# Kernel tuning notes

Measured on AMD Instinct MI355X. Metric: run time of the kernel, lower is better.

## Reference

```python
import jax, jax.numpy as jnp
import numpy as np

N, K, D, VOCAB = 20000, 32, 128, 100000
NEG = -1e30  # finite large-negative so all-masked rows don't produce NaN softmax


def setup_inputs() -> dict:
    key = jax.random.key(0)
    ks = jax.random.split(key, 10)
    return {
        "nodes": jax.random.randint(ks[0], (N,), 0, VOCAB),
        "neigh_idx": jax.random.randint(ks[1], (N, K), 0, VOCAB),
        "neigh_len": jax.random.randint(ks[2], (N,), 0, K + 1),
        "u2e": jax.random.normal(ks[3], (VOCAB, D), dtype=jnp.float32),
        "W1": jax.random.normal(ks[4], (D, 2 * D), dtype=jnp.float32) * 0.05,
        "b1": jax.random.normal(ks[5], (D,), dtype=jnp.float32) * 0.05,
        "W2": jax.random.normal(ks[6], (D, D), dtype=jnp.float32) * 0.05,
        "b2": jax.random.normal(ks[7], (D,), dtype=jnp.float32) * 0.05,
        "W3": jax.random.normal(ks[8], (1, D), dtype=jnp.float32) * 0.05,
        "b3": jax.random.normal(ks[9], (1,), dtype=jnp.float32) * 0.05,
    }


def reference(nodes, neigh_idx, neigh_len, u2e, W1, b1, W2, b2, W3, b3):
    # self features: [N, D]
    self_feats = u2e[nodes]
    # neighbor features gather: [N, K, D]
    e_u = u2e[neigh_idx]
    # GraphRec Attention: cat(neighbor, self-broadcast) -> MLP -> softmax over K
    x = jnp.concatenate(
        [e_u, jnp.broadcast_to(self_feats[:, None, :], e_u.shape)], axis=-1
    )  # [N, K, 2D]
    h = jax.nn.relu(jnp.einsum("nkf,df->nkd", x, W1) + b1)
    h = jax.nn.relu(jnp.einsum("nkd,ed->nke", h, W2) + b2)
    logits = jnp.einsum("nkd,od->nko", h, W3)[..., 0] + b3[0]  # [N, K]
    mask = jnp.arange(K)[None, :] < neigh_len[:, None]  # [N, K]
    att = jax.nn.softmax(jnp.where(mask, logits, NEG), axis=1)
    att = jnp.where(mask, att, 0.0)  # zero out padded slots (and all-empty rows)
    # attention-weighted neighbor aggregation: [N, D]
    agg = jnp.einsum("nk,nkd->nd", att, e_u)
    has_neigh = (neigh_len > 0)[:, None]
    return jnp.where(has_neigh, (agg + self_feats) * 0.5, self_feats)
```

## Files before the change

kernel.cpp:

```cpp
#include <hip/hip_runtime.h>
#include <hip/hip_bf16.h>
#include <stdint.h>

#define KN 32
#define D  128
#define NNODES 20000
#define GRID 2500
#define ITERS 4
#define VOCAB 100000
#define SV1_BLOCKS ((NNODES + 127) / 128)

typedef __bf16 bf16;
typedef __bf16 bf16x8 __attribute__((ext_vector_type(8)));
typedef float  f32x4  __attribute__((ext_vector_type(4)));

#define CHUNK_E 520
#define EU_NODE_E (8 * CHUNK_E)
#define H_STRIDE 136

#define GL2LDS(src, dst) __builtin_amdgcn_global_load_lds(                 \
    (const __attribute__((address_space(1))) void*)(src),                  \
    (__attribute__((address_space(3))) void*)(dst), 16, 0, 0)

#define MFMA(a, b, c) __builtin_amdgcn_mfma_f32_16x16x32_bf16((a), (b), (c), 0, 0, 0)

__global__ __launch_bounds__(256) void pack_weights_kernel(
    const float* __restrict__ W1, const float* __restrict__ W2,
    bf16* __restrict__ w1p, bf16* __restrict__ w2p)
{
    int t = blockIdx.x * 256 + threadIdx.x;
    if (t < 32768) {
        int j = t & 7, lane = (t >> 3) & 63, kt = (t >> 9) & 7, nt = t >> 12;
        int d = nt * 16 + (lane & 15);
        int f = kt * 32 + ((lane >> 4) << 3) + j;
        w1p[t] = (bf16)W1[d * 256 + f];
    } else if (t < 49152) {
        int u = t - 32768;
        int j = u & 7, lane = (u >> 3) & 63, kt = (u >> 9) & 3, nt = u >> 11;
        int e  = nt * 16 + (lane & 15);
        int dd = kt * 32 + ((lane >> 4) << 3) + j;
        w2p[u] = (bf16)W2[e * 128 + dd];
    }
}

__global__ __launch_bounds__(256) void convert_table_kernel(
    const float* __restrict__ u2e, bf16* __restrict__ tbl)
{
    size_t i = ((size_t)blockIdx.x * 256 + threadIdx.x) * 8;
    float4 a = *(const float4*)(u2e + i);
    float4 b = *(const float4*)(u2e + i + 4);
    bf16x8 v;
    v[0]=(bf16)a.x; v[1]=(bf16)a.y; v[2]=(bf16)a.z; v[3]=(bf16)a.w;
    v[4]=(bf16)b.x; v[5]=(bf16)b.y; v[6]=(bf16)b.z; v[7]=(bf16)b.w;
    *(bf16x8*)(tbl + i) = v;
}

__global__ __launch_bounds__(256) void sv1_kernel(
    const int*  __restrict__ nodes,
    const bf16* __restrict__ u2e_bf,
    const bf16* __restrict__ w1p,
    float*      __restrict__ sv1t)
{
    __shared__ alignas(16) bf16 sr[4 * EU_NODE_E];

    const int t    = threadIdx.x;
    const int lane = t & 63;
    const int wave = t >> 6;
    const int ln15 = lane & 15;
    const int quad = lane >> 4;
    const int r0   = blockIdx.x * 128;

    #pragma unroll
    for (int c = 0; c < 8; ++c) {
        int grow = r0 + wave * 32 + c + ((lane >> 4) << 3);
        int node = nodes[grow < NNODES ? grow : NNODES - 1];
        GL2LDS(u2e_bf + (size_t)node * D + ((lane & 15) << 3),
               sr + wave * EU_NODE_E + c * CHUNK_E);
    }
    __syncthreads();

    const bf16* g  = sr + wave * EU_NODE_E;
    const int   rb = (ln15 & 7) * CHUNK_E + (ln15 >> 3) * 128;

    #pragma unroll 1
    for (int np = 0; np < 4; ++np) {
        int nt0 = np * 2;
        bf16x8 b0[4], b1[4];
        #pragma unroll
        for (int kt = 0; kt < 4; ++kt) {
            b0[kt] = *(const bf16x8*)(w1p + (nt0 * 8 + 4 + kt) * 512 + lane * 8);
            b1[kt] = *(const bf16x8*)(w1p + ((nt0 + 1) * 8 + 4 + kt) * 512 + lane * 8);
        }
        f32x4 c00 = {0.f,0.f,0.f,0.f}, c01 = c00, c10 = c00, c11 = c00;
        #pragma unroll
        for (int kt = 0; kt < 4; ++kt) {
            bf16x8 a0 = *(const bf16x8*)(g + rb + kt * 32 + quad * 8);
            bf16x8 a1 = *(const bf16x8*)(g + rb + 256 + kt * 32 + quad * 8);
            c00 = MFMA(a0, b0[kt], c00);
            c01 = MFMA(a0, b1[kt], c01);
            c10 = MFMA(a1, b0[kt], c10);
            c11 = MFMA(a1, b1[kt], c11);
        }
        #pragma unroll
        for (int r = 0; r < 4; ++r) {
            int row = quad * 4 + r;
            int gr0 = r0 + wave * 32 + row;
            int gr1 = gr0 + 16;
            if (gr0 < NNODES) {
                sv1t[(size_t)gr0 * D + nt0 * 16 + ln15]       = c00[r];
                sv1t[(size_t)gr0 * D + (nt0 + 1) * 16 + ln15] = c01[r];
            }
            if (gr1 < NNODES) {
                sv1t[(size_t)gr1 * D + nt0 * 16 + ln15]       = c10[r];
                sv1t[(size_t)gr1 * D + (nt0 + 1) * 16 + ln15] = c11[r];
            }
        }
    }
}

__global__ __launch_bounds__(256, 4) void graphrec_agg_kernel(
    const int*   __restrict__ nodes,
    const int*   __restrict__ neigh_idx,
    const int*   __restrict__ neigh_len,
    const float* __restrict__ u2e,
    const bf16*  __restrict__ u2e_bf,
    const float* __restrict__ sv1t,
    const float* __restrict__ b1,
    const float* __restrict__ b2,
    const float* __restrict__ W3,
    const float* __restrict__ b3,
    const bf16*  __restrict__ w1p,
    const bf16*  __restrict__ w2p,
    float*       __restrict__ out)
{
    __shared__ alignas(16) bf16  eu[2 * EU_NODE_E];
    __shared__ alignas(16) float self_f[2 * D];
    __shared__ alignas(16) bf16  h1[2 * KN * H_STRIDE];
    __shared__ float lpart[2][4 * KN];

    const int t    = threadIdx.x;
    const int lane = t & 63;
    const int wave = t >> 6;
    const int ln15 = lane & 15;
    const int quad = lane >> 4;
    const int nt0  = wave * 2;

    const float bias1_0 = b1[nt0 * 16 + ln15];
    const float bias1_1 = b1[(nt0 + 1) * 16 + ln15];
    const float bias2_0 = b2[nt0 * 16 + ln15];
    const float bias2_1 = b2[(nt0 + 1) * 16 + ln15];
    const float w3_0    = W3[nt0 * 16 + ln15];
    const float w3_1    = W3[(nt0 + 1) * 16 + ln15];
    const float b3v     = b3[0];

    bf16x8 w1r[2][4];
    #pragma unroll
    for (int nt = 0; nt < 2; ++nt)
        #pragma unroll
        for (int ft = 0; ft < 4; ++ft)
            w1r[nt][ft] = *(const bf16x8*)(w1p + ((nt0 + nt) * 8 + ft) * 512 + lane * 8);
    bf16x8 w2r[2][4];
    #pragma unroll
    for (int nt = 0; nt < 2; ++nt)
        #pragma unroll
        for (int kt = 0; kt < 4; ++kt)
            w2r[nt][kt] = *(const bf16x8*)(w2p + ((nt0 + nt) * 4 + kt) * 512 + lane * 8);

    #pragma unroll 1
    for (int it = 0; it < ITERS; ++it) {
        const int nA   = blockIdx.x * 8 + it * 2;
        const int lenA = neigh_len[nA];
        const int lenB = neigh_len[nA + 1];

        const float svA0 = sv1t[(size_t)nA * D + nt0 * 16 + ln15];
        const float svA1 = sv1t[(size_t)nA * D + (nt0 + 1) * 16 + ln15];
        const float svB0 = sv1t[(size_t)(nA + 1) * D + nt0 * 16 + ln15];
        const float svB1 = sv1t[(size_t)(nA + 1) * D + (nt0 + 1) * 16 + ln15];

        {
            const int gnd = wave >> 1;
            const int cb  = (wave & 1) * 4;
            #pragma unroll
            for (int j = 0; j < 4; ++j) {
                int chunk = cb + j;
                int idx = neigh_idx[(nA + gnd) * KN + chunk + ((lane >> 4) << 3)];
                GL2LDS(u2e_bf + (size_t)idx * D + ((lane & 15) << 3),
                       eu + gnd * EU_NODE_E + chunk * CHUNK_E);
            }
            if (wave == 0) {
                int sidx = nodes[nA + (lane >> 5)];
                GL2LDS(u2e + (size_t)sidx * D + ((lane & 31) << 2), self_f);
            }
        }
        __syncthreads();

        #pragma unroll 1
        for (int nd = 0; nd < 2; ++nd) {
            const bf16* euN = eu + nd * EU_NODE_E;
            bf16* h1N = h1 + nd * KN * H_STRIDE;

            f32x4 c00 = {0.f,0.f,0.f,0.f}, c01 = c00, c10 = c00, c11 = c00;
            const int rb = (ln15 & 7) * CHUNK_E + (ln15 >> 3) * 128;
            #pragma unroll
            for (int ft = 0; ft < 4; ++ft) {
                bf16x8 a0 = *(const bf16x8*)(euN + rb + ft * 32 + quad * 8);
                bf16x8 a1 = *(const bf16x8*)(euN + rb + 256 + ft * 32 + quad * 8);
                c00 = MFMA(a0, w1r[0][ft], c00);
                c01 = MFMA(a0, w1r[1][ft], c01);
                c10 = MFMA(a1, w1r[0][ft], c10);
                c11 = MFMA(a1, w1r[1][ft], c11);
            }
            const float s0 = nd ? svB0 : svA0;
            const float s1 = nd ? svB1 : svA1;
            #pragma unroll
            for (int r = 0; r < 4; ++r) {
                int row = quad * 4 + r;
                h1N[row * H_STRIDE + nt0 * 16 + ln15]              = (bf16)fmaxf(c00[r] + bias1_0 + s0, 0.f);
                h1N[row * H_STRIDE + (nt0 + 1) * 16 + ln15]        = (bf16)fmaxf(c01[r] + bias1_1 + s1, 0.f);
                h1N[(16 + row) * H_STRIDE + nt0 * 16 + ln15]       = (bf16)fmaxf(c10[r] + bias1_0 + s0, 0.f);
                h1N[(16 + row) * H_STRIDE + (nt0 + 1) * 16 + ln15] = (bf16)fmaxf(c11[r] + bias1_1 + s1, 0.f);
            }
        }
        __syncthreads();

        #pragma unroll 1
        for (int nd = 0; nd < 2; ++nd) {
            const bf16* h1N = h1 + nd * KN * H_STRIDE;
            f32x4 d00 = {0.f,0.f,0.f,0.f}, d01 = d00, d10 = d00, d11 = d00;
            #pragma unroll
            for (int kt = 0; kt < 4; ++kt) {
                bf16x8 a0 = *(const bf16x8*)(h1N + ln15 * H_STRIDE + kt * 32 + quad * 8);
                bf16x8 a1 = *(const bf16x8*)(h1N + (16 + ln15) * H_STRIDE + kt * 32 + quad * 8);
                d00 = MFMA(a0, w2r[0][kt], d00);
                d01 = MFMA(a0, w2r[1][kt], d01);
                d10 = MFMA(a1, w2r[0][kt], d10);
                d11 = MFMA(a1, w2r[1][kt], d11);
            }
            #pragma unroll
            for (int r = 0; r < 4; ++r) {
                float p0 = w3_0 * fmaxf(d00[r] + bias2_0, 0.f)
                         + w3_1 * fmaxf(d01[r] + bias2_1, 0.f);
                float p1 = w3_0 * fmaxf(d10[r] + bias2_0, 0.f)
                         + w3_1 * fmaxf(d11[r] + bias2_1, 0.f);
                #pragma unroll
                for (int o = 1; o < 16; o <<= 1) {
                    p0 += __shfl_xor(p0, o);
                    p1 += __shfl_xor(p1, o);
                }
                if (ln15 == 0) {
                    lpart[nd][wave * KN + quad * 4 + r]      = p0;
                    lpart[nd][wave * KN + 16 + quad * 4 + r] = p1;
                }
            }
        }
        __syncthreads();

        {
            const int nd = wave >> 1;
            const int k  = lane & 31;
            float lg = lpart[nd][k] + lpart[nd][KN + k] + lpart[nd][2 * KN + k]
                     + lpart[nd][3 * KN + k] + b3v;
            const int len = nd ? lenB : lenA;
            bool act = k < len;
            float l = act ? lg : -1e30f;
            float m = l;
            #pragma unroll
            for (int o = 1; o < 32; o <<= 1) m = fmaxf(m, __shfl_xor(m, o));
            float e = act ? expf(l - m) : 0.f;
            float s = e;
            #pragma unroll
            for (int o = 1; o < 32; o <<= 1) s += __shfl_xor(s, o);
            float att = (s > 0.f) ? (e / s) : 0.f;

            const int d = ((wave & 1) << 6) + lane;
            const bf16* euN = eu + nd * EU_NODE_E;
            float acc = 0.f;
            #pragma unroll
            for (int k2 = 0; k2 < KN; ++k2) {
                float a  = __shfl(att, k2);
                float ev = (float)euN[(k2 & 7) * CHUNK_E + (k2 >> 3) * 128 + (d & 127)];
                acc += a * ev;
            }
            float sf = self_f[nd * D + (d & 127)];
            out[(size_t)(nA + nd) * D + (d & 127)] = (len > 0) ? 0.5f * (acc + sf) : sf;
        }
        __syncthreads();
    }
}

#define FB_CHUNK_DW 260
#define FB_EU_NODE_DW (16 * FB_CHUNK_DW)

__global__ __launch_bounds__(256, 3) void graphrec_agg_fb(
    const int*   __restrict__ nodes,
    const int*   __restrict__ neigh_idx,
    const int*   __restrict__ neigh_len,
    const float* __restrict__ u2e,
    const float* __restrict__ b1,
    const float* __restrict__ b2,
    const float* __restrict__ W3,
    const float* __restrict__ b3,
    const bf16*  __restrict__ w1p,
    const bf16*  __restrict__ w2p,
    float*       __restrict__ out)
{
    __shared__ alignas(16) float eu[2 * FB_EU_NODE_DW];
    __shared__ alignas(16) bf16  h1[2 * KN * H_STRIDE];
    __shared__ alignas(16) float self_f[2 * D];
    __shared__ float lpart[2][4 * KN];
    __shared__ float att_s[2][KN];

    const int t    = threadIdx.x;
    const int lane = t & 63;
    const int wave = t >> 6;
    const int ln15 = lane & 15;
    const int quad = lane >> 4;
    const int nt0  = wave * 2;

    const float bias1_0 = b1[nt0 * 16 + ln15];
    const float bias1_1 = b1[(nt0 + 1) * 16 + ln15];
    const float bias2_0 = b2[nt0 * 16 + ln15];
    const float bias2_1 = b2[(nt0 + 1) * 16 + ln15];
    const float w3_0    = W3[nt0 * 16 + ln15];
    const float w3_1    = W3[(nt0 + 1) * 16 + ln15];
    const float b3v     = b3[0];

    bf16x8 w1r[2][8];
    #pragma unroll
    for (int nt = 0; nt < 2; ++nt)
        #pragma unroll
        for (int ft = 0; ft < 8; ++ft)
            w1r[nt][ft] = *(const bf16x8*)(w1p + ((nt0 + nt) * 8 + ft) * 512 + lane * 8);
    bf16x8 w2r[2][4];
    #pragma unroll
    for (int nt = 0; nt < 2; ++nt)
        #pragma unroll
        for (int kt = 0; kt < 4; ++kt)
            w2r[nt][kt] = *(const bf16x8*)(w2p + ((nt0 + nt) * 4 + kt) * 512 + lane * 8);

    #pragma unroll 1
    for (int it = 0; it < ITERS; ++it) {
        const int nA   = blockIdx.x * 8 + it * 2;
        const int lenA = neigh_len[nA];
        const int lenB = neigh_len[nA + 1];
        {
            const int half = lane >> 5;
            const int colb = (lane & 31) << 4;
            #pragma unroll
            for (int nd = 0; nd < 2; ++nd) {
                #pragma unroll
                for (int j = 0; j < 4; ++j) {
                    int chunk = wave * 4 + j;
                    int idx = neigh_idx[(nA + nd) * KN + chunk + (half << 4)];
                    const char* src = (const char*)(u2e + (size_t)idx * D) + colb;
                    GL2LDS(src, eu + nd * FB_EU_NODE_DW + chunk * FB_CHUNK_DW);
                }
            }
            if (wave == 0) {
                int sidx = nodes[nA + half];
                const char* src = (const char*)(u2e + (size_t)sidx * D) + colb;
                GL2LDS(src, self_f);
            }
        }
        __syncthreads();
        #pragma unroll 1
        for (int nd = 0; nd < 2; ++nd) {
            const float* euN = eu + nd * FB_EU_NODE_DW;
            const float* sfN = self_f + nd * D;
            bf16* h1N = h1 + nd * KN * H_STRIDE;
            f32x4 c00 = {0.f,0.f,0.f,0.f}, c01 = c00, c10 = c00, c11 = c00;
            const int r0 = ln15 * FB_CHUNK_DW;
            #pragma unroll
            for (int ft = 0; ft < 4; ++ft) {
                int off = ft * 32 + quad * 8;
                f32x4 u0 = *(const f32x4*)(euN + r0 + off);
                f32x4 u1 = *(const f32x4*)(euN + r0 + off + 4);
                f32x4 v0 = *(const f32x4*)(euN + r0 + 128 + off);
                f32x4 v1 = *(const f32x4*)(euN + r0 + 128 + off + 4);
                bf16x8 a0, a1;
                #pragma unroll
                for (int e = 0; e < 4; ++e) {
                    a0[e] = (bf16)u0[e]; a0[4 + e] = (bf16)u1[e];
                    a1[e] = (bf16)v0[e]; a1[4 + e] = (bf16)v1[e];
                }
                c00 = MFMA(a0, w1r[0][ft], c00);
                c01 = MFMA(a0, w1r[1][ft], c01);
                c10 = MFMA(a1, w1r[0][ft], c10);
                c11 = MFMA(a1, w1r[1][ft], c11);
            }
            #pragma unroll
            for (int ft = 4; ft < 8; ++ft) {
                int off = (ft - 4) * 32 + quad * 8;
                f32x4 u0 = *(const f32x4*)(sfN + off);
                f32x4 u1 = *(const f32x4*)(sfN + off + 4);
                bf16x8 a;
                #pragma unroll
                for (int e = 0; e < 4; ++e) { a[e] = (bf16)u0[e]; a[4 + e] = (bf16)u1[e]; }
                c00 = MFMA(a, w1r[0][ft], c00);
                c01 = MFMA(a, w1r[1][ft], c01);
                c10 = MFMA(a, w1r[0][ft], c10);
                c11 = MFMA(a, w1r[1][ft], c11);
            }
            #pragma unroll
            for (int r = 0; r < 4; ++r) {
                int row = quad * 4 + r;
                h1N[row * H_STRIDE + nt0 * 16 + ln15]              = (bf16)fmaxf(c00[r] + bias1_0, 0.f);
                h1N[row * H_STRIDE + (nt0 + 1) * 16 + ln15]        = (bf16)fmaxf(c01[r] + bias1_1, 0.f);
                h1N[(16 + row) * H_STRIDE + nt0 * 16 + ln15]       = (bf16)fmaxf(c10[r] + bias1_0, 0.f);
                h1N[(16 + row) * H_STRIDE + (nt0 + 1) * 16 + ln15] = (bf16)fmaxf(c11[r] + bias1_1, 0.f);
            }
        }
        __syncthreads();
        #pragma unroll 1
        for (int nd = 0; nd < 2; ++nd) {
            const bf16* h1N = h1 + nd * KN * H_STRIDE;
            f32x4 d00 = {0.f,0.f,0.f,0.f}, d01 = d00, d10 = d00, d11 = d00;
            #pragma unroll
            for (int kt = 0; kt < 4; ++kt) {
                bf16x8 a0 = *(const bf16x8*)(h1N + ln15 * H_STRIDE + kt * 32 + quad * 8);
                bf16x8 a1 = *(const bf16x8*)(h1N + (16 + ln15) * H_STRIDE + kt * 32 + quad * 8);
                d00 = MFMA(a0, w2r[0][kt], d00);
                d01 = MFMA(a0, w2r[1][kt], d01);
                d10 = MFMA(a1, w2r[0][kt], d10);
                d11 = MFMA(a1, w2r[1][kt], d11);
            }
            #pragma unroll
            for (int r = 0; r < 4; ++r) {
                float p0 = w3_0 * fmaxf(d00[r] + bias2_0, 0.f)
                         + w3_1 * fmaxf(d01[r] + bias2_1, 0.f);
                float p1 = w3_0 * fmaxf(d10[r] + bias2_0, 0.f)
                         + w3_1 * fmaxf(d11[r] + bias2_1, 0.f);
                #pragma unroll
                for (int o = 1; o < 16; o <<= 1) {
                    p0 += __shfl_xor(p0, o);
                    p1 += __shfl_xor(p1, o);
                }
                if (ln15 == 0) {
                    lpart[nd][wave * KN + quad * 4 + r]      = p0;
                    lpart[nd][wave * KN + 16 + quad * 4 + r] = p1;
                }
            }
        }
        __syncthreads();
        if (wave < 2) {
            int nd = wave, k = lane & 31;
            float lg = lpart[nd][k] + lpart[nd][KN + k] + lpart[nd][2 * KN + k]
                     + lpart[nd][3 * KN + k] + b3v;
            int len = nd ? lenB : lenA;
            bool act = (lane < 32) && (k < len);
            float l = act ? lg : -1e30f;
            float m = l;
            #pragma unroll
            for (int o = 1; o < 32; o <<= 1) m = fmaxf(m, __shfl_xor(m, o));
            float e = act ? expf(l - m) : 0.f;
            float s = e;
            #pragma unroll
            for (int o = 1; o < 32; o <<= 1) s += __shfl_xor(s, o);
            if (lane < 32) att_s[nd][k] = (s > 0.f) ? (e / s) : 0.f;
        }
        __syncthreads();
        {
            int nd = t >> 7, d = t & 127;
            const float* euN = eu + nd * FB_EU_NODE_DW;
            float acc = 0.f;
            #pragma unroll
            for (int k = 0; k < KN; ++k)
                acc += att_s[nd][k] * euN[(k & 15) * FB_CHUNK_DW + ((k >> 4) << 7) + d];
            float sf = self_f[nd * D + d];
            int len = nd ? lenB : lenA;
            out[(size_t)(nA + nd) * D + d] = (len > 0) ? 0.5f * (acc + sf) : sf;
        }
        __syncthreads();
    }
}

extern "C" void kernel_launch(void* const* d_in, const int* in_sizes, int n_in,
                              void* d_out, int out_size, void* d_ws, size_t ws_size,
                              hipStream_t stream) {
    const int*   nodes     = (const int*)d_in[0];
    const int*   neigh_idx = (const int*)d_in[1];
    const int*   neigh_len = (const int*)d_in[2];
    const float* u2e       = (const float*)d_in[3];
    const float* W1        = (const float*)d_in[4];
    const float* b1        = (const float*)d_in[5];
    const float* W2        = (const float*)d_in[6];
    const float* b2        = (const float*)d_in[7];
    const float* W3        = (const float*)d_in[8];
    const float* b3        = (const float*)d_in[9];
    float* out = (float*)d_out;

    bf16*  w1p    = (bf16*)d_ws;
    bf16*  w2p    = w1p + 32768;
    bf16*  u2e_bf = (bf16*)((char*)d_ws + 98304);
    float* sv1t   = (float*)((char*)d_ws + 98304 + (size_t)VOCAB * D * 2);
    const size_t need = 98304ull + (size_t)VOCAB * D * 2 + (size_t)NNODES * D * 4;

    pack_weights_kernel<<<192, 256, 0, stream>>>(W1, W2, w1p, w2p);
    if (ws_size >= need) {
        convert_table_kernel<<<VOCAB * D / 2048, 256, 0, stream>>>(u2e, u2e_bf);
        sv1_kernel<<<SV1_BLOCKS, 256, 0, stream>>>(nodes, u2e_bf, w1p, sv1t);
        graphrec_agg_kernel<<<GRID, 256, 0, stream>>>(nodes, neigh_idx, neigh_len,
                                                      u2e, u2e_bf, sv1t, b1, b2,
                                                      W3, b3, w1p, w2p, out);
    } else {
        graphrec_agg_fb<<<GRID, 256, 0, stream>>>(nodes, neigh_idx, neigh_len, u2e,
                                                  b1, b2, W3, b3, w1p, w2p, out);
    }
}
```

Before: 215.9 us.

## Merge preprocessing kernels into one launch and vectorize the attention aggregation

Folds the table conversion, weight packing and self-feature projection into a single aux kernel that partitions its grid by block index. The self projection now reads fp32 rows and W1 straight from global memory, so it no longer depends on the other two outputs and can run alongside them. The aggregation step in the main kernel switches to 8-wide bf16 vector LDS reads with a shuffle reduction across neighbor groups and vectorized output stores. This removes two launches and their serialization, at the cost of fp32 W1 reloads per wave in the projection.

```diff
diff --git a/kernel.cpp b/kernel.cpp
--- a/kernel.cpp
+++ b/kernel.cpp
@@ -8,7 +8,11 @@
 #define GRID 2500
 #define ITERS 4
 #define VOCAB 100000
-#define SV1_BLOCKS ((NNODES + 127) / 128)
+
+#define CONV_BLOCKS 6250
+#define PACK_BLOCKS 192
+#define SV1_BLOCKS  ((NNODES + 63) / 64)
+#define AUX_BLOCKS  (CONV_BLOCKS + PACK_BLOCKS + SV1_BLOCKS)
 
 typedef __bf16 bf16;
 typedef __bf16 bf16x8 __attribute__((ext_vector_type(8)));
@@ -17,6 +21,7 @@
 #define CHUNK_E 520
 #define EU_NODE_E (8 * CHUNK_E)
 #define H_STRIDE 136
+#define CHUNK_DW 260
 
 #define GL2LDS(src, dst) __builtin_amdgcn_global_load_lds(                 \
     (const __attribute__((address_space(1))) void*)(src),                  \
@@ -24,95 +29,124 @@
 
 #define MFMA(a, b, c) __builtin_amdgcn_mfma_f32_16x16x32_bf16((a), (b), (c), 0, 0, 0)
 
-__global__ __launch_bounds__(256) void pack_weights_kernel(
-    const float* __restrict__ W1, const float* __restrict__ W2,
-    bf16* __restrict__ w1p, bf16* __restrict__ w2p)
+__global__ __launch_bounds__(256) void aux_kernel(
+    const float* __restrict__ u2e,
+    const float* __restrict__ W1,
+    const float* __restrict__ W2,
+    const int*   __restrict__ nodes,
+    bf16*  __restrict__ u2e_bf,
+    bf16*  __restrict__ w1p,
+    bf16*  __restrict__ w2p,
+    float* __restrict__ sv1t)
 {
-    int t = blockIdx.x * 256 + threadIdx.x;
-    if (t < 32768) {
-        int j = t & 7, lane = (t >> 3) & 63, kt = (t >> 9) & 7, nt = t >> 12;
-        int d = nt * 16 + (lane & 15);
-        int f = kt * 32 + ((lane >> 4) << 3) + j;
-        w1p[t] = (bf16)W1[d * 256 + f];
-    } else if (t < 49152) {
-        int u = t - 32768;
-        int j = u & 7, lane = (u >> 3) & 63, kt = (u >> 9) & 3, nt = u >> 11;
-        int e  = nt * 16 + (lane & 15);
-        int dd = kt * 32 + ((lane >> 4) << 3) + j;
-        w2p[u] = (bf16)W2[e * 128 + dd];
-    }
-}
-
-__global__ __launch_bounds__(256) void convert_table_kernel(
-    const float* __restrict__ u2e, bf16* __restrict__ tbl)
-{
-    size_t i = ((size_t)blockIdx.x * 256 + threadIdx.x) * 8;
-    float4 a = *(const float4*)(u2e + i);
-    float4 b = *(const float4*)(u2e + i + 4);
-    bf16x8 v;
-    v[0]=(bf16)a.x; v[1]=(bf16)a.y; v[2]=(bf16)a.z; v[3]=(bf16)a.w;
-    v[4]=(bf16)b.x; v[5]=(bf16)b.y; v[6]=(bf16)b.z; v[7]=(bf16)b.w;
-    *(bf16x8*)(tbl + i) = v;
-}
-
-__global__ __launch_bounds__(256) void sv1_kernel(
-    const int*  __restrict__ nodes,
-    const bf16* __restrict__ u2e_bf,
-    const bf16* __restrict__ w1p,
-    float*      __restrict__ sv1t)
-{
-    __shared__ alignas(16) bf16 sr[4 * EU_NODE_E];
-
-    const int t    = threadIdx.x;
-    const int lane = t & 63;
-    const int wave = t >> 6;
-    const int ln15 = lane & 15;
-    const int quad = lane >> 4;
-    const int r0   = blockIdx.x * 128;
-
-    #pragma unroll
-    for (int c = 0; c < 8; ++c) {
-        int grow = r0 + wave * 32 + c + ((lane >> 4) << 3);
-        int node = nodes[grow < NNODES ? grow : NNODES - 1];
-        GL2LDS(u2e_bf + (size_t)node * D + ((lane & 15) << 3),
-               sr + wave * EU_NODE_E + c * CHUNK_E);
-    }
-    __syncthreads();
-
-    const bf16* g  = sr + wave * EU_NODE_E;
-    const int   rb = (ln15 & 7) * CHUNK_E + (ln15 >> 3) * 128;
-
-    #pragma unroll 1
-    for (int np = 0; np < 4; ++np) {
-        int nt0 = np * 2;
-        bf16x8 b0[4], b1[4];
-        #pragma unroll
-        for (int kt = 0; kt < 4; ++kt) {
-            b0[kt] = *(const bf16x8*)(w1p + (nt0 * 8 + 4 + kt) * 512 + lane * 8);
-            b1[kt] = *(const bf16x8*)(w1p + ((nt0 + 1) * 8 + 4 + kt) * 512 + lane * 8);
-        }
-        f32x4 c00 = {0.f,0.f,0.f,0.f}, c01 = c00, c10 = c00, c11 = c00;
-        #pragma unroll
-        for (int kt = 0; kt < 4; ++kt) {
-            bf16x8 a0 = *(const bf16x8*)(g + rb + kt * 32 + quad * 8);
-            bf16x8 a1 = *(const bf16x8*)(g + rb + 256 + kt * 32 + quad * 8);
-            c00 = MFMA(a0, b0[kt], c00);
-            c01 = MFMA(a0, b1[kt], c01);
-            c10 = MFMA(a1, b0[kt], c10);
-            c11 = MFMA(a1, b1[kt], c11);
-        }
-        #pragma unroll
-        for (int r = 0; r < 4; ++r) {
-            int row = quad * 4 + r;
-            int gr0 = r0 + wave * 32 + row;
-            int gr1 = gr0 + 16;
-            if (gr0 < NNODES) {
-                sv1t[(size_t)gr0 * D + nt0 * 16 + ln15]       = c00[r];
-                sv1t[(size_t)gr0 * D + (nt0 + 1) * 16 + ln15] = c01[r];
-            }
-            if (gr1 < NNODES) {
-                sv1t[(size_t)gr1 * D + nt0 * 16 + ln15]       = c10[r];
-                sv1t[(size_t)gr1 * D + (nt0 + 1) * 16 + ln15] = c11[r];
+    const int b = blockIdx.x;
+    const int t = threadIdx.x;
+
+    if (b < CONV_BLOCKS) {
+        size_t i = ((size_t)b * 256 + t) * 8;
+        float4 a = *(const float4*)(u2e + i);
+        float4 c = *(const float4*)(u2e + i + 4);
+        bf16x8 v;
+        v[0]=(bf16)a.x; v[1]=(bf16)a.y; v[2]=(bf16)a.z; v[3]=(bf16)a.w;
+        v[4]=(bf16)c.x; v[5]=(bf16)c.y; v[6]=(bf16)c.z; v[7]=(bf16)c.w;
+        *(bf16x8*)(u2e_bf + i) = v;
+        return;
+    }
+    if (b < CONV_BLOCKS + PACK_BLOCKS) {
+        int g = (b - CONV_BLOCKS) * 256 + t;
+        if (g < 32768) {
+            int j = g & 7, lane = (g >> 3) & 63, kt = (g >> 9) & 7, nt = g >> 12;
+            int d = nt * 16 + (lane & 15);
+            int f = kt * 32 + ((lane >> 4) << 3) + j;
+            w1p[g] = (bf16)W1[d * 256 + f];
+        } else if (g < 49152) {
+            int u = g - 32768;
+            int j = u & 7, lane = (u >> 3) & 63, kt = (u >> 9) & 3, nt = u >> 11;
+            int e  = nt * 16 + (lane & 15);
+            int dd = kt * 32 + ((lane >> 4) << 3) + j;
+            w2p[u] = (bf16)W2[e * 128 + dd];
+        }
+        return;
+    }
+    {
+        __shared__ alignas(16) float sr[2 * 16 * CHUNK_DW];
+
+        const int sb   = b - CONV_BLOCKS - PACK_BLOCKS;
+        const int base = sb * 64;
+        const int lane = t & 63;
+        const int wave = t >> 6;
+        const int ln15 = lane & 15;
+        const int quad = lane >> 4;
+
+        {
+            const int grp  = wave & 1;
+            const int cb   = (wave >> 1) * 8;
+            const int half = lane >> 5;
+            const int colb = (lane & 31) << 4;
+            #pragma unroll
+            for (int j = 0; j < 8; ++j) {
+                int chunk = cb + j;
+                int row = base + grp * 32 + chunk + half * 16;
+                int node = nodes[row < NNODES ? row : NNODES - 1];
+                GL2LDS((const char*)(u2e + (size_t)node * D) + colb,
+                       sr + grp * 16 * CHUNK_DW + chunk * CHUNK_DW);
+            }
+        }
+        __syncthreads();
+
+        const float* g  = sr + (wave & 1) * 16 * CHUNK_DW;
+        const int    r0 = ln15 * CHUNK_DW;
+
+        #pragma unroll 1
+        for (int np = (wave >> 1) * 2; np <= (wave >> 1) * 2 + 1; ++np) {
+            const int nt0 = np * 2;
+            bf16x8 b0[4], b1[4];
+            #pragma unroll
+            for (int kt = 0; kt < 4; ++kt) {
+                const float* s0 = W1 + (size_t)(nt0 * 16 + ln15) * 256 + 128 + kt * 32 + quad * 8;
+                const float* s1 = W1 + (size_t)((nt0 + 1) * 16 + ln15) * 256 + 128 + kt * 32 + quad * 8;
+                f32x4 u0 = *(const f32x4*)(s0), u1 = *(const f32x4*)(s0 + 4);
+                f32x4 v0 = *(const f32x4*)(s1), v1 = *(const f32x4*)(s1 + 4);
+                bf16x8 bb0, bb1;
+                #pragma unroll
+                for (int e = 0; e < 4; ++e) {
+                    bb0[e] = (bf16)u0[e]; bb0[4 + e] = (bf16)u1[e];
+                    bb1[e] = (bf16)v0[e]; bb1[4 + e] = (bf16)v1[e];
+                }
+                b0[kt] = bb0; b1[kt] = bb1;
+            }
+            f32x4 c00 = {0.f,0.f,0.f,0.f}, c01 = c00, c10 = c00, c11 = c00;
+            #pragma unroll
+            for (int kt = 0; kt < 4; ++kt) {
+                int off = kt * 32 + quad * 8;
+                f32x4 u0 = *(const f32x4*)(g + r0 + off);
+                f32x4 u1 = *(const f32x4*)(g + r0 + off + 4);
+                f32x4 v0 = *(const f32x4*)(g + r0 + 128 + off);
+                f32x4 v1 = *(const f32x4*)(g + r0 + 128 + off + 4);
+                bf16x8 a0, a1;
+                #pragma unroll
+                for (int e = 0; e < 4; ++e) {
+                    a0[e] = (bf16)u0[e]; a0[4 + e] = (bf16)u1[e];
+                    a1[e] = (bf16)v0[e]; a1[4 + e] = (bf16)v1[e];
+                }
+                c00 = MFMA(a0, b0[kt], c00);
+                c01 = MFMA(a0, b1[kt], c01);
+                c10 = MFMA(a1, b0[kt], c10);
+                c11 = MFMA(a1, b1[kt], c11);
+            }
+            #pragma unroll
+            for (int r = 0; r < 4; ++r) {
+                int row = quad * 4 + r;
+                int gr0 = base + (wave & 1) * 32 + row;
+                int gr1 = gr0 + 16;
+                if (gr0 < NNODES) {
+                    sv1t[(size_t)gr0 * D + nt0 * 16 + ln15]       = c00[r];
+                    sv1t[(size_t)gr0 * D + (nt0 + 1) * 16 + ln15] = c01[r];
+                }
+                if (gr1 < NNODES) {
+                    sv1t[(size_t)gr1 * D + nt0 * 16 + ln15]       = c10[r];
+                    sv1t[(size_t)gr1 * D + (nt0 + 1) * 16 + ln15] = c11[r];
+                }
             }
         }
     }
@@ -256,8 +290,12 @@
         __syncthreads();
 
         {
-            const int nd = wave >> 1;
-            const int k  = lane & 31;
+            const int nd    = wave >> 1;
+            const int dbase = (wave & 1) * 64;
+            const int g     = lane >> 3;
+            const int l3    = lane & 7;
+            const int k     = lane & 31;
+
             float lg = lpart[nd][k] + lpart[nd][KN + k] + lpart[nd][2 * KN + k]
                      + lpart[nd][3 * KN + k] + b3v;
             const int len = nd ? lenB : lenA;
@@ -272,24 +310,61 @@
             for (int o = 1; o < 32; o <<= 1) s += __shfl_xor(s, o);
             float att = (s > 0.f) ? (e / s) : 0.f;
 
-            const int d = ((wave & 1) << 6) + lane;
             const bf16* euN = eu + nd * EU_NODE_E;
-            float acc = 0.f;
-            #pragma unroll
-            for (int k2 = 0; k2 < KN; ++k2) {
-                float a  = __shfl(att, k2);
-                float ev = (float)euN[(k2 & 7) * CHUNK_E + (k2 >> 3) * 128 + (d & 127)];
-                acc += a * ev;
-            }
-            float sf = self_f[nd * D + (d & 127)];
-            out[(size_t)(nA + nd) * D + (d & 127)] = (len > 0) ? 0.5f * (acc + sf) : sf;
+            float acc[8] = {0.f,0.f,0.f,0.f,0.f,0.f,0.f,0.f};
+            #pragma unroll
+            for (int p = 0; p < 4; ++p) {
+                int kk = p * 8 + g;
+                float attk = __shfl(att, kk);
+                bf16x8 v = *(const bf16x8*)(euN + g * CHUNK_E + p * 128 + dbase + l3 * 8);
+                #pragma unroll
+                for (int j = 0; j < 8; ++j) acc[j] += attk * (float)v[j];
+            }
+            #pragma unroll
+            for (int j = 0; j < 8; ++j) {
+                acc[j] += __shfl_xor(acc[j], 8);
+                acc[j] += __shfl_xor(acc[j], 16);
+                acc[j] += __shfl_xor(acc[j], 32);
+            }
+            if (g == 0) {
+                const float* sfp = self_f + nd * D + dbase + l3 * 8;
+                f32x4 sf0 = *(const f32x4*)(sfp);
+                f32x4 sf1 = *(const f32x4*)(sfp + 4);
+                f32x4 o0, o1;
+                #pragma unroll
+                for (int j = 0; j < 4; ++j) {
+                    o0[j] = (len > 0) ? 0.5f * (acc[j] + sf0[j])     : sf0[j];
+                    o1[j] = (len > 0) ? 0.5f * (acc[4 + j] + sf1[j]) : sf1[j];
+                }
+                float* op = out + (size_t)(nA + nd) * D + dbase + l3 * 8;
+                *(f32x4*)(op)     = o0;
+                *(f32x4*)(op + 4) = o1;
+            }
         }
         __syncthreads();
     }
 }
 
-#define FB_CHUNK_DW 260
-#define FB_EU_NODE_DW (16 * FB_CHUNK_DW)
+#define FB_EU_NODE_DW (16 * CHUNK_DW)
+
+__global__ __launch_bounds__(256) void pack_weights_kernel(
+    const float* __restrict__ W1, const float* __restrict__ W2,
+    bf16* __restrict__ w1p, bf16* __restrict__ w2p)
+{
+    int t = blockIdx.x * 256 + threadIdx.x;
+    if (t < 32768) {
+        int j = t & 7, lane = (t >> 3) & 63, kt = (t >> 9) & 7, nt = t >> 12;
+        int d = nt * 16 + (lane & 15);
+        int f = kt * 32 + ((lane >> 4) << 3) + j;
+        w1p[t] = (bf16)W1[d * 256 + f];
+    } else if (t < 49152) {
+        int u = t - 32768;
+        int j = u & 7, lane = (u >> 3) & 63, kt = (u >> 9) & 3, nt = u >> 11;
+        int e  = nt * 16 + (lane & 15);
+        int dd = kt * 32 + ((lane >> 4) << 3) + j;
+        w2p[u] = (bf16)W2[e * 128 + dd];
+    }
+}
 
 __global__ __launch_bounds__(256, 3) void graphrec_agg_fb(
     const int*   __restrict__ nodes,
@@ -353,7 +428,7 @@
                     int chunk = wave * 4 + j;
                     int idx = neigh_idx[(nA + nd) * KN + chunk + (half << 4)];
                     const char* src = (const char*)(u2e + (size_t)idx * D) + colb;
-                    GL2LDS(src, eu + nd * FB_EU_NODE_DW + chunk * FB_CHUNK_DW);
+                    GL2LDS(src, eu + nd * FB_EU_NODE_DW + chunk * CHUNK_DW);
                 }
             }
             if (wave == 0) {
@@ -369,7 +444,7 @@
             const float* sfN = self_f + nd * D;
             bf16* h1N = h1 + nd * KN * H_STRIDE;
             f32x4 c00 = {0.f,0.f,0.f,0.f}, c01 = c00, c10 = c00, c11 = c00;
-            const int r0 = ln15 * FB_CHUNK_DW;
+            const int r0 = ln15 * CHUNK_DW;
             #pragma unroll
             for (int ft = 0; ft < 4; ++ft) {
                 int off = ft * 32 + quad * 8;
@@ -465,7 +540,7 @@
             float acc = 0.f;
             #pragma unroll
             for (int k = 0; k < KN; ++k)
-                acc += att_s[nd][k] * euN[(k & 15) * FB_CHUNK_DW + ((k >> 4) << 7) + d];
+                acc += att_s[nd][k] * euN[(k & 15) * CHUNK_DW + ((k >> 4) << 7) + d];
             float sf = self_f[nd * D + d];
             int len = nd ? lenB : lenA;
             out[(size_t)(nA + nd) * D + d] = (len > 0) ? 0.5f * (acc + sf) : sf;
@@ -495,14 +570,14 @@
     float* sv1t   = (float*)((char*)d_ws + 98304 + (size_t)VOCAB * D * 2);
     const size_t need = 98304ull + (size_t)VOCAB * D * 2 + (size_t)NNODES * D * 4;
 
-    pack_weights_kernel<<<192, 256, 0, stream>>>(W1, W2, w1p, w2p);
     if (ws_size >= need) {
-        convert_table_kernel<<<VOCAB * D / 2048, 256, 0, stream>>>(u2e, u2e_bf);
-        sv1_kernel<<<SV1_BLOCKS, 256, 0, stream>>>(nodes, u2e_bf, w1p, sv1t);
+        aux_kernel<<<AUX_BLOCKS, 256, 0, stream>>>(u2e, W1, W2, nodes,
+                                                   u2e_bf, w1p, w2p, sv1t);
         graphrec_agg_kernel<<<GRID, 256, 0, stream>>>(nodes, neigh_idx, neigh_len,
                                                       u2e, u2e_bf, sv1t, b1, b2,
                                                       W3, b3, w1p, w2p, out);
     } else {
+        pack_weights_kernel<<<192, 256, 0, stream>>>(W1, W2, w1p, w2p);
         graphrec_agg_fb<<<GRID, 256, 0, stream>>>(nodes, neigh_idx, neigh_len, u2e,
                                                   b1, b2, W3, b3, w1p, w2p, out);
     }
```

After: 223.1 us. 1.03x slower.
